# Performance work log

Hardware: AMD Instinct MI355X
Metric: run time of the kernel (lower is better)

The kernel has to match this reference:

```python
import jax, jax.numpy as jnp
import numpy as np

V, N, D, R, L, KS = 32000, 2048, 1024, 16, 4, 7
B, H = 2, 4 * 1024
GMIN, GMAX, ACAP = 0.85, 1.0, 1.0


def rmsnorm(x, w, eps=1e-6):
    return x * jax.lax.rsqrt(jnp.mean(x * x, axis=-1, keepdims=True) + eps) * w


def l2norm(x, eps=1e-8):
    return x / jnp.maximum(jnp.linalg.norm(x, axis=-1, keepdims=True), eps)


def mlp(x, w1, b1, w2, b2):
    return jax.nn.gelu(x @ w1 + b1) @ w2 + b2


def k1_block(h, nw, w1, b1, w2, b2):
    return h + mlp(rmsnorm(h, nw), w1, b1, w2, b2)


def causal_conv(h, kernel):
    # depthwise causal conv with shared 1D kernel; kernel[0] = current step
    n = h.shape[1]
    hp = jnp.pad(h, ((0, 0), (KS - 1, 0), (0, 0)))
    out = jnp.zeros_like(h)
    for k in range(KS):  # KS is small & static
        out = out + kernel[k] * hp[:, KS - 1 - k: KS - 1 - k + n, :]
    return out


def k2_layer(h, p):
    (u, v, dlog, alog, glog, kern, pw, pb, n1w, n2w, w1, b1, w2, b2) = p
    residual = h
    hn = rmsnorm(h, n1w)
    gate = jax.nn.sigmoid(glog)
    out = gate * causal_conv(hn, kern)
    # low-rank q/k
    q = l2norm(hn @ u)          # (B,N,R)
    k = l2norm(hn @ v)          # (B,N,R)
    gamma = GMIN + (GMAX - GMIN) * jax.nn.sigmoid(dlog)   # (R,)
    alpha = ACAP * jax.nn.sigmoid(alog)                   # (R,)
    qa = q * alpha
    pos = jnp.arange(h.shape[1])
    diff = jnp.maximum(pos[:, None] - pos[None, :], 0).astype(h.dtype)
    mask = (pos[:, None] >= pos[None, :]).astype(h.dtype)
    # per-rank causal decay matrix gamma_r^(i-j): (R,N,N)
    decay = jnp.exp(diff[None] * jnp.log(gamma)[:, None, None]) * mask[None]
    scores = jnp.einsum('bir,rij,bjr->bij', qa, decay, k)  # (B,N,N)
    out = out + jnp.einsum('bij,bjd->bid', scores, hn)
    out = out @ pw + pb
    h = residual + out
    h = h + mlp(rmsnorm(h, n2w), w1, b1, w2, b2)
    return h


def setup_inputs() -> dict:
    key = jax.random.key(0)
    ks = jax.random.split(key, 32)
    f32 = jnp.float32
    inp = {
        'tokens': jax.random.randint(ks[0], (B, N), 0, V),
        'emb_table': jax.random.normal(ks[1], (V, D), f32) * 0.02,
        'k1a_nw': jnp.ones((D,), f32),
        'k1a_w1': jax.random.normal(ks[2], (D, H), f32) * 0.02,
        'k1a_b1': jnp.zeros((H,), f32),
        'k1a_w2': jax.random.normal(ks[3], (H, D), f32) * 0.02,
        'k1a_b2': jnp.zeros((D,), f32),
        'k2_u': jax.random.normal(ks[4], (L, D, R), f32) * 0.05,
        'k2_v': jax.random.normal(ks[5], (L, D, R), f32) * 0.05,
        'k2_dlog': jax.random.normal(ks[6], (L, R), f32) * 0.5,
        'k2_alog': jnp.zeros((L, R), f32),
        'k2_glog': jnp.zeros((L,), f32),
        'k2_kern': jax.random.normal(ks[7], (L, KS), f32) * 0.1,
        'k2_pw': jax.random.normal(ks[8], (L, D, D), f32) * 0.02,
        'k2_pb': jnp.zeros((L, D), f32),
        'k2_n1w': jnp.ones((L, D), f32),
        'k2_n2w': jnp.ones((L, D), f32),
        'k2_w1': jax.random.normal(ks[9], (L, D, H), f32) * 0.02,
        'k2_b1': jnp.zeros((L, H), f32),
        'k2_w2': jax.random.normal(ks[10], (L, H, D), f32) * 0.02,
        'k2_b2': jnp.zeros((L, D), f32),
        'k1b_nw': jnp.ones((D,), f32),
        'k1b_w1': jax.random.normal(ks[11], (D, H), f32) * 0.02,
        'k1b_b1': jnp.zeros((H,), f32),
        'k1b_w2': jax.random.normal(ks[12], (H, D), f32) * 0.02,
        'k1b_b2': jnp.zeros((D,), f32),
        'k0_nw': jnp.ones((D,), f32),
        'head_w': jax.random.normal(ks[13], (D, V), f32) * 0.02,
        'head_b': jnp.zeros((V,), f32),
    }
    return inp


def reference(tokens, emb_table,
              k1a_nw, k1a_w1, k1a_b1, k1a_w2, k1a_b2,
              k2_u, k2_v, k2_dlog, k2_alog, k2_glog, k2_kern,
              k2_pw, k2_pb, k2_n1w, k2_n2w, k2_w1, k2_b1, k2_w2, k2_b2,
              k1b_nw, k1b_w1, k1b_b1, k1b_w2, k1b_b2,
              k0_nw, head_w, head_b):
    h = emb_table[tokens]                                  # (B,N,D)
    h = k1_block(h, k1a_nw, k1a_w1, k1a_b1, k1a_w2, k1a_b2)
    stacked = (k2_u, k2_v, k2_dlog, k2_alog, k2_glog, k2_kern,
               k2_pw, k2_pb, k2_n1w, k2_n2w, k2_w1, k2_b1, k2_w2, k2_b2)
    def step(c, p):
        return k2_layer(c, p), None
    h, _ = jax.lax.scan(step, h, stacked)
    h = k1_block(h, k1b_nw, k1b_w1, k1b_b1, k1b_w2, k1b_b2)
    h = rmsnorm(h, k0_nw)                                  # K0 final norm
    return h @ head_w + head_b                             # (B,N,V)
```

## Files before the change

### kernel.cpp

```cpp
#include <hip/hip_runtime.h>
#include <hip/hip_bf16.h>

#define SEQ 2048
#define DIM 1024
#define RNK 16
#define NL 4
#define KT 7
#define BATCH 2
#define HID 4096
#define VOC 32000
#define BNROWS (BATCH*SEQ)
#define CHK 128
#define NCH (SEQ/CHK)
#define PRMS 128
#define KAPP 160

typedef __hip_bfloat16 bf16;
typedef __attribute__((ext_vector_type(8))) short bh8;
typedef __attribute__((ext_vector_type(4))) float vf4;

__device__ __forceinline__ float bfu(unsigned int u) { u <<= 16; return __builtin_bit_cast(float, u); }
__device__ __forceinline__ unsigned short f2bu(float x) { bf16 t = __float2bfloat16(x); return __builtin_bit_cast(unsigned short, t); }
__device__ __forceinline__ float b2f(bf16 x) { return __bfloat162float(x); }
__device__ __forceinline__ float sigm(float x) { return 1.f / (1.f + expf(-x)); }
__device__ __forceinline__ float gelu_t(float x) {
    float u = 0.7978845608028654f * (x + 0.044715f * x * x * x);
    return 0.5f * x * (1.f + tanhf(u));
}

__device__ __forceinline__ void gld16(const bf16* g, bf16* l) {
    __builtin_amdgcn_global_load_lds(
        (const __attribute__((address_space(1))) void*)g,
        (__attribute__((address_space(3))) void*)l,
        16, 0, 0);
}

__global__ void embed_kernel(const int* __restrict__ tokens, const float* __restrict__ emb,
                             float* __restrict__ h) {
    int row = blockIdx.x;
    int tok = tokens[row];
    const float4* src = (const float4*)(emb + (size_t)tok * DIM);
    float4* dst = (float4*)(h + (size_t)row * DIM);
    dst[threadIdx.x] = src[threadIdx.x];
}

__global__ void rmsnorm_kernel(const float* __restrict__ in, const float* __restrict__ wt,
                               bf16* __restrict__ out) {
    int row = blockIdx.x;
    int tx = threadIdx.x;
    float4 v = ((const float4*)(in + (size_t)row * DIM))[tx];
    float ss = v.x * v.x + v.y * v.y + v.z * v.z + v.w * v.w;
#pragma unroll
    for (int off = 32; off > 0; off >>= 1) ss += __shfl_down(ss, off);
    __shared__ float red[4];
    int lane = tx & 63, wv = tx >> 6;
    if (lane == 0) red[wv] = ss;
    __syncthreads();
    float tot = red[0] + red[1] + red[2] + red[3];
    float scale = rsqrtf(tot * (1.f / DIM) + 1e-6f);
    float4 w4 = ((const float4*)wt)[tx];
    uint2 o;
    o.x = f2bu(v.x * scale * w4.x) | ((unsigned int)f2bu(v.y * scale * w4.y) << 16);
    o.y = f2bu(v.z * scale * w4.z) | ((unsigned int)f2bu(v.w * scale * w4.w) << 16);
    *(uint2*)(out + (size_t)row * DIM + tx * 4) = o;
}

__global__ void transpose_cast_kernel(const float* __restrict__ in, bf16* __restrict__ out,
                                      int K, int Nc) {
    __shared__ float tile[32][33];
    int n0 = blockIdx.x * 32, k0 = blockIdx.y * 32;
    int tx = threadIdx.x & 31, ty = threadIdx.x >> 5;
#pragma unroll
    for (int i = 0; i < 32; i += 8)
        tile[ty + i][tx] = in[(size_t)(k0 + ty + i) * Nc + n0 + tx];
    __syncthreads();
#pragma unroll
    for (int i = 0; i < 32; i += 8)
        out[(size_t)(n0 + ty + i) * K + k0 + tx] = __float2bfloat16(tile[tx][ty + i]);
}

__global__ void prep_kernel(const float* __restrict__ dlog, const float* __restrict__ alog,
                            const float* __restrict__ glog, const float* __restrict__ kern,
                            float* __restrict__ prm) {
    int l = blockIdx.x, t = threadIdx.x;
    float* p = prm + l * PRMS;
    if (t < RNK) {
        float g = 0.85f + 0.15f * sigm(dlog[l * RNK + t]);
        float lg = logf(g);
        p[t] = g;
        p[16 + t] = lg;
        p[32 + t] = expf(lg * (float)CHK);
        p[48 + t] = sigm(alog[l * RNK + t]);
    }
    if (t < KT) {
        float gate = sigm(glog[l]);
        p[64 + t] = gate * kern[l * KT + t];
    }
}

__global__ void prep_uv_kernel(const float* __restrict__ u, const float* __restrict__ v,
                               bf16* __restrict__ uvT) {
    int l = blockIdx.y;
    int k = blockIdx.x * 256 + threadIdx.x;
    const float* ul = u + (size_t)l * DIM * RNK;
    const float* vl = v + (size_t)l * DIM * RNK;
    bf16* o = uvT + (size_t)l * 32 * DIM;
#pragma unroll
    for (int r = 0; r < RNK; ++r) {
        o[(size_t)r * DIM + k] = __float2bfloat16(ul[(size_t)k * RNK + r]);
        o[(size_t)(RNK + r) * DIM + k] = __float2bfloat16(vl[(size_t)k * RNK + r]);
    }
}

__global__ void conv_kernel(const bf16* __restrict__ hn, const float* __restrict__ prm,
                            float* __restrict__ Z) {
    int t = blockIdx.x * 256 + threadIdx.x;
    int d4 = (t & 255) * 4;
    int row = t >> 8;
    int n = row & (SEQ - 1);
    float a0 = 0, a1 = 0, a2 = 0, a3 = 0;
#pragma unroll
    for (int kk = 0; kk < KT; ++kk) {
        if (n - kk < 0) break;
        float wv = prm[64 + kk];
        uint2 hv = *(const uint2*)(hn + (size_t)(row - kk) * DIM + d4);
        a0 += wv * bfu(hv.x & 0xffffu);
        a1 += wv * bfu(hv.x >> 16);
        a2 += wv * bfu(hv.y & 0xffffu);
        a3 += wv * bfu(hv.y >> 16);
    }
    float4 o = {a0, a1, a2, a3};
    *(float4*)(Z + (size_t)row * DIM + d4) = o;
}

__global__ __launch_bounds__(64)
void qk_mfma_kernel(const bf16* __restrict__ hn, const bf16* __restrict__ uvT,
                    const float* __restrict__ prm, float* __restrict__ qa,
                    float* __restrict__ kn) {
    int row0 = blockIdx.x * 32;
    int lane = threadIdx.x;
    int fr = lane & 15, kf = (lane >> 4) * 8;
    vf4 acc[2][2] = {};
#pragma unroll 4
    for (int kt = 0; kt < DIM / 32; ++kt) {
        int k0 = kt * 32;
        bh8 b0 = *(const bh8*)(uvT + (size_t)fr * DIM + k0 + kf);
        bh8 b1 = *(const bh8*)(uvT + (size_t)(16 + fr) * DIM + k0 + kf);
        bh8 a0 = *(const bh8*)(hn + (size_t)(row0 + fr) * DIM + k0 + kf);
        bh8 a1 = *(const bh8*)(hn + (size_t)(row0 + 16 + fr) * DIM + k0 + kf);
        acc[0][0] = __builtin_amdgcn_mfma_f32_16x16x32_bf16(a0, b0, acc[0][0], 0, 0, 0);
        acc[0][1] = __builtin_amdgcn_mfma_f32_16x16x32_bf16(a0, b1, acc[0][1], 0, 0, 0);
        acc[1][0] = __builtin_amdgcn_mfma_f32_16x16x32_bf16(a1, b0, acc[1][0], 0, 0, 0);
        acc[1][1] = __builtin_amdgcn_mfma_f32_16x16x32_bf16(a1, b1, acc[1][1], 0, 0, 0);
    }
    int fq = lane >> 4;
    float alpha = prm[48 + fr];
#pragma unroll
    for (int m = 0; m < 2; ++m) {
#pragma unroll
        for (int j = 0; j < 4; ++j) {
            float qv = acc[m][0][j], kv = acc[m][1][j];
            float sq = qv * qv, sk = kv * kv;
#pragma unroll
            for (int mask = 1; mask < 16; mask <<= 1) {
                sq += __shfl_xor(sq, mask);
                sk += __shfl_xor(sk, mask);
            }
            int row = row0 + m * 16 + fq * 4 + j;
            qa[(size_t)row * RNK + fr] = qv / fmaxf(sqrtf(sq), 1e-8f) * alpha;
            kn[(size_t)row * RNK + fr] = kv / fmaxf(sqrtf(sk), 1e-8f);
        }
    }
}

__global__ void trans_hn_kernel(const bf16* __restrict__ hn, bf16* __restrict__ HB) {
    __shared__ bf16 tile[32][40];
    int bc = blockIdx.x;
    int d0 = blockIdx.y * 32, j0 = blockIdx.z * 32;
    int tx = threadIdx.x & 31, ty = threadIdx.x >> 5;
    size_t rowb = (size_t)bc * CHK;
#pragma unroll
    for (int i = 0; i < 32; i += 8)
        tile[ty + i][tx] = hn[(rowb + j0 + ty + i) * DIM + d0 + tx];
    __syncthreads();
    bf16* Hp = HB + (size_t)bc * DIM * KAPP;
#pragma unroll
    for (int i = 0; i < 32; i += 8)
        Hp[(size_t)(d0 + ty + i) * KAPP + j0 + tx] = tile[tx][ty + i];
}

__global__ void scores_kernel(const float* __restrict__ qa, const float* __restrict__ kn,
                              const float* __restrict__ prm, bf16* __restrict__ SA,
                              bf16* __restrict__ kdtB) {
    int bc = blockIdx.x;
    __shared__ float ptab[CHK][16];
    for (int e = threadIdx.x; e < CHK * 16; e += 256) {
        int tt = e >> 4, r = e & 15;
        ptab[tt][r] = expf(prm[16 + r] * (float)tt);
    }
    __syncthreads();
    size_t rowb = (size_t)bc * CHK;
    bf16* SAp = SA + (size_t)bc * CHK * KAPP;
    for (int e = threadIdx.x; e < CHK * CHK; e += 256) {
        int i = e >> 7, j = e & (CHK - 1);
        float vsum = 0.f;
        if (i >= j) {
            const float* qp = qa + (rowb + i) * RNK;
            const float* kp = kn + (rowb + j) * RNK;
#pragma unroll
            for (int r = 0; r < 16; ++r) vsum += qp[r] * ptab[i - j][r] * kp[r];
        }
        SAp[(size_t)i * KAPP + j] = __float2bfloat16(vsum);
    }
    for (int e = threadIdx.x; e < CHK * 32; e += 256) {
        int i = e >> 5, rr = e & 31;
        float w = 0.f;
        if (rr < 16) w = qa[(rowb + i) * RNK + rr] * expf(prm[16 + rr] * (float)(i + 1));
        SAp[(size_t)i * KAPP + CHK + rr] = __float2bfloat16(w);
    }
    bf16* kp2 = kdtB + (size_t)bc * RNK * CHK;
    for (int e = threadIdx.x; e < RNK * CHK; e += 256) {
        int r = e >> 7, j = e & (CHK - 1);
        kp2[e] = __float2bfloat16(ptab[CHK - 1 - j][r] * kn[(rowb + j) * RNK + r]);
    }
}

__global__ __launch_bounds__(64)
void chunkU_kernel(const bf16* __restrict__ HB, const bf16* __restrict__ kdtB,
                   float* __restrict__ U) {
    int bc = blockIdx.x;
    int d0 = blockIdx.y * 64;
    int lane = threadIdx.x;
    int fr = lane & 15, kf = (lane >> 4) * 8;
    const bf16* Hp = HB + (size_t)bc * DIM * KAPP;
    const bf16* Kp = kdtB + (size_t)bc * RNK * CHK;
    vf4 acc[4] = {};
#pragma unroll
    for (int kt = 0; kt < 4; ++kt) {
        int k0 = kt * 32;
        bh8 bb = *(const bh8*)(Kp + (size_t)fr * CHK + k0 + kf);
#pragma unroll
        for (int m = 0; m < 4; ++m) {
            bh8 a = *(const bh8*)(Hp + (size_t)(d0 + m * 16 + fr) * KAPP + k0 + kf);
            acc[m] = __builtin_amdgcn_mfma_f32_16x16x32_bf16(a, bb, acc[m], 0, 0, 0);
        }
    }
    int fq = lane >> 4;
    float* Up = U + (size_t)bc * DIM * RNK;
#pragma unroll
    for (int m = 0; m < 4; ++m)
#pragma unroll
        for (int j = 0; j < 4; ++j)
            Up[(size_t)(d0 + m * 16 + fq * 4 + j) * RNK + fr] = acc[m][j];
}

__global__ void scanP_kernel(const float* __restrict__ U, const float* __restrict__ prm,
                             bf16* __restrict__ HB) {
    int g = blockIdx.x * 256 + threadIdx.x;
    int d = g & (DIM - 1);
    int b = g >> 10;
    float gC[16], p[16];
#pragma unroll
    for (int r = 0; r < 16; ++r) { gC[r] = prm[32 + r]; p[r] = 0.f; }
    for (int c = 0; c < NCH; ++c) {
        int bc = b * NCH + c;
        unsigned int pk[8];
#pragma unroll
        for (int q = 0; q < 8; ++q)
            pk[q] = (unsigned int)f2bu(p[2 * q]) | ((unsigned int)f2bu(p[2 * q + 1]) << 16);
        uint4* dst = (uint4*)(HB + (size_t)bc * DIM * KAPP + (size_t)d * KAPP + CHK);
        dst[0] = make_uint4(pk[0], pk[1], pk[2], pk[3]);
        dst[1] = make_uint4(pk[4], pk[5], pk[6], pk[7]);
        const float4* up = (const float4*)(U + ((size_t)bc * DIM + d) * RNK);
#pragma unroll
        for (int q = 0; q < 4; ++q) {
            float4 u4 = up[q];
            p[4 * q + 0] = gC[4 * q + 0] * p[4 * q + 0] + u4.x;
            p[4 * q + 1] = gC[4 * q + 1] * p[4 * q + 1] + u4.y;
            p[4 * q + 2] = gC[4 * q + 2] * p[4 * q + 2] + u4.z;
            p[4 * q + 3] = gC[4 * q + 3] * p[4 * q + 3] + u4.w;
        }
    }
}

__global__ __launch_bounds__(256)
void apply_gemm_kernel(const bf16* __restrict__ SA, const bf16* __restrict__ HB,
                       const float* __restrict__ Z, bf16* __restrict__ Zb) {
    __shared__ alignas(16) bf16 As[128][40];
    __shared__ alignas(16) bf16 Bs[128][40];
    int bc = blockIdx.y;
    int colB0 = blockIdx.x * 128;
    int t = threadIdx.x;
    int lane = t & 63, wid = t >> 6;
    int wr = wid >> 1, wc = wid & 1;
    vf4 acc[4][4] = {};
    const bf16* A = SA + (size_t)bc * CHK * KAPP;
    const bf16* BT = HB + (size_t)bc * DIM * KAPP;
    int r1 = t >> 2, ko1 = (t & 3) * 8;
    int fr = lane & 15, kf = (lane >> 4) * 8;
#pragma unroll
    for (int kt = 0; kt < 5; ++kt) {
        int k0 = kt * 32;
        int4 va1 = *(const int4*)(A + (size_t)r1 * KAPP + k0 + ko1);
        int4 va2 = *(const int4*)(A + (size_t)(r1 + 64) * KAPP + k0 + ko1);
        int4 vb1 = *(const int4*)(BT + (size_t)(colB0 + r1) * KAPP + k0 + ko1);
        int4 vb2 = *(const int4*)(BT + (size_t)(colB0 + r1 + 64) * KAPP + k0 + ko1);
        __syncthreads();
        *(int4*)&As[r1][ko1] = va1;
        *(int4*)&As[r1 + 64][ko1] = va2;
        *(int4*)&Bs[r1][ko1] = vb1;
        *(int4*)&Bs[r1 + 64][ko1] = vb2;
        __syncthreads();
        bh8 a[4], bb[4];
#pragma unroll
        for (int m = 0; m < 4; ++m) a[m] = *(const bh8*)&As[wr * 64 + m * 16 + fr][kf];
#pragma unroll
        for (int n = 0; n < 4; ++n) bb[n] = *(const bh8*)&Bs[wc * 64 + n * 16 + fr][kf];
#pragma unroll
        for (int m = 0; m < 4; ++m)
#pragma unroll
            for (int n = 0; n < 4; ++n)
                acc[m][n] = __builtin_amdgcn_mfma_f32_16x16x32_bf16(a[m], bb[n], acc[m][n], 0, 0, 0);
    }
    int fq = lane >> 4;
    size_t rowb = (size_t)bc * CHK;
#pragma unroll
    for (int m = 0; m < 4; ++m) {
#pragma unroll
        for (int n = 0; n < 4; ++n) {
            int col = colB0 + wc * 64 + n * 16 + fr;
#pragma unroll
            for (int j = 0; j < 4; ++j) {
                size_t row = rowb + wr * 64 + m * 16 + fq * 4 + j;
                size_t idx = row * DIM + col;
                Zb[idx] = __float2bfloat16(Z[idx] + acc[m][n][j]);
            }
        }
    }
}

template <int EPI>
__global__ __launch_bounds__(256)
void gemm_kernel(const bf16* __restrict__ A, const bf16* __restrict__ BT,
                 const float* __restrict__ bias, const float* __restrict__ res,
                 float* __restrict__ outF, bf16* __restrict__ outB,
                 int M, int Nc, int K, int lda) {
    __shared__ alignas(16) bf16 As[128][32];
    __shared__ alignas(16) bf16 Bs[128][32];
    int gx = gridDim.x;
    int orig = blockIdx.y * gx + blockIdx.x;
    int qch = (gx * gridDim.y) >> 3;
    int wg = (orig & 7) * qch + (orig >> 3);
    int bn = wg % gx, bm = wg / gx;
    int t = threadIdx.x;
    int lane = t & 63, wid = t >> 6;
    int wr = wid >> 1, wc = wid & 1;
    vf4 acc[4][4] = {};
    const int rowA0 = bm * 128, colB0 = bn * 128;
    int fr = lane & 15, kf = (lane >> 4) * 8;
    int c0 = wid * 2;
    int lrow = lane >> 2;
    int lcol = (lane & 3) * 8;
    const bf16* Ag0 = A + (size_t)(rowA0 + c0 * 16 + lrow) * lda + lcol;
    const bf16* Ag1 = A + (size_t)(rowA0 + c0 * 16 + 16 + lrow) * lda + lcol;
    const bf16* Bg0 = BT + (size_t)(colB0 + c0 * 16 + lrow) * lda + lcol;
    const bf16* Bg1 = BT + (size_t)(colB0 + c0 * 16 + 16 + lrow) * lda + lcol;
    bf16* Al0 = &As[0][0] + c0 * 512;
    bf16* Al1 = Al0 + 512;
    bf16* Bl0 = &Bs[0][0] + c0 * 512;
    bf16* Bl1 = Bl0 + 512;
    int nk = K >> 5;
    for (int kt = 0; kt < nk; ++kt) {
        int k0 = kt * 32;
        __syncthreads();
        gld16(Ag0 + k0, Al0);
        gld16(Ag1 + k0, Al1);
        gld16(Bg0 + k0, Bl0);
        gld16(Bg1 + k0, Bl1);
        asm volatile("s_waitcnt vmcnt(0)" ::: "memory");
        __syncthreads();
        bh8 a[4], bb[4];
#pragma unroll
        for (int m = 0; m < 4; ++m) a[m] = *(const bh8*)&As[wr * 64 + m * 16 + fr][kf];
#pragma unroll
        for (int n = 0; n < 4; ++n) bb[n] = *(const bh8*)&Bs[wc * 64 + n * 16 + fr][kf];
#pragma unroll
        for (int m = 0; m < 4; ++m)
#pragma unroll
            for (int n = 0; n < 4; ++n)
                acc[m][n] = __builtin_amdgcn_mfma_f32_16x16x32_bf16(a[m], bb[n], acc[m][n], 0, 0, 0);
    }
    int fq = lane >> 4;
#pragma unroll
    for (int m = 0; m < 4; ++m) {
#pragma unroll
        for (int n = 0; n < 4; ++n) {
            int col = colB0 + wc * 64 + n * 16 + fr;
            float bv = bias[col];
#pragma unroll
            for (int j = 0; j < 4; ++j) {
                int row = rowA0 + wr * 64 + m * 16 + fq * 4 + j;
                size_t idx = (size_t)row * Nc + col;
                float v2 = acc[m][n][j] + bv;
                if (EPI == 1) v2 += res[idx];
                outF[idx] = v2;
            }
        }
    }
}

#define SB __builtin_amdgcn_sched_barrier(0)
template <int EPI>
__global__ __launch_bounds__(512, 2)
void gemm256_kernel(const bf16* __restrict__ A, const bf16* __restrict__ BT,
                    const float* __restrict__ bias,
                    float* __restrict__ outF, bf16* __restrict__ outB,
                    int M, int Nc, int K, int lda) {
    extern __shared__ char smem[];
    bf16* Alds = (bf16*)smem;
    bf16* Blds = (bf16*)(smem + 65536);
    if (EPI == 3) {
        size_t zo = (size_t)blockIdx.z * K;
        A += zo; BT += zo;
        outF += (size_t)blockIdx.z * ((size_t)M * Nc);
    }
    int gx = gridDim.x, gy = gridDim.y;
    int orig = blockIdx.y * gx + blockIdx.x;
    int qch = (gx * gy) >> 3;
    int wg = (orig & 7) * qch + (orig >> 3);
    int bm = wg % gy, bn = wg / gy;
    int rowA0 = bm * 256, colB0 = bn * 256;
    int tid = threadIdx.x;
    int lane = tid & 63, wid = tid >> 6;
    int wm = wid >> 2, wn = wid & 3;
    int fr = lane & 15;
    int kf8 = ((((lane >> 4) & 3) ^ ((fr >> 1) & 3)) * 8);
    int srow = wid * 16 + (lane >> 2);
    int scol = (((lane & 3) ^ ((lane >> 3) & 3)) * 8);
    const bf16* Ags = A + (size_t)(rowA0 + srow) * lda + scol;
    const bf16* Bgs = BT + (size_t)(colB0 + srow) * lda + scol;
    int sbase = wid * 512;
    auto stA = [&](int d, int kh, int k0) {
        bf16* dst = Alds + (d * 2 + kh) * 8192 + sbase;
        const bf16* src = Ags + k0 + kh * 32;
        gld16(src, dst);
        gld16(src + (size_t)128 * lda, dst + 4096);
    };
    auto stB = [&](int d, int kh, int k0) {
        bf16* dst = Blds + (d * 2 + kh) * 8192 + sbase;
        const bf16* src = Bgs + k0 + kh * 32;
        gld16(src, dst);
        gld16(src + (size_t)128 * lda, dst + 4096);
    };
    const bf16* Ard = Alds + (size_t)(wm * 128 + fr) * 32 + kf8;
    const bf16* Brd = Blds + (size_t)(wn * 64 + fr) * 32 + kf8;
    vf4 acc[8][4] = {};
    int nt = K >> 6;
    stA(0, 0, 0); stB(0, 0, 0); stA(0, 1, 0); stB(0, 1, 0);
    for (int t = 0; t < nt; ++t) {
        int d = t & 1, nd = d ^ 1;
        int k1 = (t + 1) << 6;
        bool pf = (t + 1 < nt);
        int dof = d * 16384;
        bh8 bF[4];
        if (pf) { stA(nd, 0, k1); asm volatile("s_waitcnt vmcnt(6)" ::: "memory"); }
        else    {                 asm volatile("s_waitcnt vmcnt(4)" ::: "memory"); }
        SB; __builtin_amdgcn_s_barrier(); SB;
        {
            bh8 a0 = *(const bh8*)(Ard + dof + 0 * 512);
            bh8 a1 = *(const bh8*)(Ard + dof + 1 * 512);
            bh8 a2 = *(const bh8*)(Ard + dof + 2 * 512);
            bh8 a3 = *(const bh8*)(Ard + dof + 3 * 512);
#pragma unroll
            for (int n = 0; n < 4; ++n) bF[n] = *(const bh8*)(Brd + dof + n * 512);
            __builtin_amdgcn_s_setprio(1);
#pragma unroll
            for (int n = 0; n < 4; ++n) {
                acc[0][n] = __builtin_amdgcn_mfma_f32_16x16x32_bf16(a0, bF[n], acc[0][n], 0, 0, 0);
                acc[1][n] = __builtin_amdgcn_mfma_f32_16x16x32_bf16(a1, bF[n], acc[1][n], 0, 0, 0);
                acc[2][n] = __builtin_amdgcn_mfma_f32_16x16x32_bf16(a2, bF[n], acc[2][n], 0, 0, 0);
                acc[3][n] = __builtin_amdgcn_mfma_f32_16x16x32_bf16(a3, bF[n], acc[3][n], 0, 0, 0);
            }
            __builtin_amdgcn_s_setprio(0);
        }
        SB;
        if (pf) stB(nd, 0, k1);
        SB; __builtin_amdgcn_s_barrier(); SB;
        {
            bh8 a0 = *(const bh8*)(Ard + dof + 4 * 512);
            bh8 a1 = *(const bh8*)(Ard + dof + 5 * 512);
            bh8 a2 = *(const bh8*)(Ard + dof + 6 * 512);
            bh8 a3 = *(const bh8*)(Ard + dof + 7 * 512);
            __builtin_amdgcn_s_setprio(1);
#pragma unroll
            for (int n = 0; n < 4; ++n) {
                acc[4][n] = __builtin_amdgcn_mfma_f32_16x16x32_bf16(a0, bF[n], acc[4][n], 0, 0, 0);
                acc[5][n] = __builtin_amdgcn_mfma_f32_16x16x32_bf16(a1, bF[n], acc[5][n], 0, 0, 0);
                acc[6][n] = __builtin_amdgcn_mfma_f32_16x16x32_bf16(a2, bF[n], acc[6][n], 0, 0, 0);
                acc[7][n] = __builtin_amdgcn_mfma_f32_16x16x32_bf16(a3, bF[n], acc[7][n], 0, 0, 0);
            }
            __builtin_amdgcn_s_setprio(0);
        }
        SB;
        int dof1 = dof + 8192;
        if (pf) { stA(nd, 1, k1); asm volatile("s_waitcnt vmcnt(6)" ::: "memory"); }
        else    {                 asm volatile("s_waitcnt vmcnt(0)" ::: "memory"); }
        SB; __builtin_amdgcn_s_barrier(); SB;
        {
            bh8 a0 = *(const bh8*)(Ard + dof1 + 0 * 512);
            bh8 a1 = *(const bh8*)(Ard + dof1 + 1 * 512);
            bh8 a2 = *(const bh8*)(Ard + dof1 + 2 * 512);
            bh8 a3 = *(const bh8*)(Ard + dof1 + 3 * 512);
#pragma unroll
            for (int n = 0; n < 4; ++n) bF[n] = *(const bh8*)(Brd + dof1 + n * 512);
            __builtin_amdgcn_s_setprio(1);
#pragma unroll
            for (int n = 0; n < 4; ++n) {
                acc[0][n] = __builtin_amdgcn_mfma_f32_16x16x32_bf16(a0, bF[n], acc[0][n], 0, 0, 0);
                acc[1][n] = __builtin_amdgcn_mfma_f32_16x16x32_bf16(a1, bF[n], acc[1][n], 0, 0, 0);
                acc[2][n] = __builtin_amdgcn_mfma_f32_16x16x32_bf16(a2, bF[n], acc[2][n], 0, 0, 0);
                acc[3][n] = __builtin_amdgcn_mfma_f32_16x16x32_bf16(a3, bF[n], acc[3][n], 0, 0, 0);
            }
            __builtin_amdgcn_s_setprio(0);
        }
        SB;
        if (pf) stB(nd, 1, k1);
        SB; __builtin_amdgcn_s_barrier(); SB;
        {
            bh8 a0 = *(const bh8*)(Ard + dof1 + 4 * 512);
            bh8 a1 = *(const bh8*)(Ard + dof1 + 5 * 512);
            bh8 a2 = *(const bh8*)(Ard + dof1 + 6 * 512);
            bh8 a3 = *(const bh8*)(Ard + dof1 + 7 * 512);
            __builtin_amdgcn_s_setprio(1);
#pragma unroll
            for (int n = 0; n < 4; ++n) {
                acc[4][n] = __builtin_amdgcn_mfma_f32_16x16x32_bf16(a0, bF[n], acc[4][n], 0, 0, 0);
                acc[5][n] = __builtin_amdgcn_mfma_f32_16x16x32_bf16(a1, bF[n], acc[5][n], 0, 0, 0);
                acc[6][n] = __builtin_amdgcn_mfma_f32_16x16x32_bf16(a2, bF[n], acc[6][n], 0, 0, 0);
                acc[7][n] = __builtin_amdgcn_mfma_f32_16x16x32_bf16(a3, bF[n], acc[7][n], 0, 0, 0);
            }
            __builtin_amdgcn_s_setprio(0);
        }
        SB;
    }
    int fq = lane >> 4;
#pragma unroll
    for (int mi = 0; mi < 8; ++mi) {
#pragma unroll
        for (int ni = 0; ni < 4; ++ni) {
            int col = colB0 + wn * 64 + ni * 16 + fr;
            float bv = (EPI == 3) ? 0.f : bias[col];
#pragma unroll
            for (int j = 0; j < 4; ++j) {
                int row = rowA0 + wm * 128 + mi * 16 + fq * 4 + j;
                size_t idx = (size_t)row * Nc + col;
                float v2 = acc[mi][ni][j] + bv;
                if (EPI == 2) outB[idx] = __float2bfloat16(gelu_t(v2));
                else outF[idx] = v2;
            }
        }
    }
}

__global__ void combine4_norm_kernel(const float* __restrict__ P, const float* __restrict__ bias,
                                     const float* __restrict__ nw, float* __restrict__ h,
                                     bf16* __restrict__ hnb) {
    int row = blockIdx.x;
    int tx = threadIdx.x;
    int t = row * 256 + tx;
    const size_t S = (size_t)BNROWS * DIM;
    float4 p0 = ((const float4*)P)[t];
    float4 p1 = ((const float4*)(P + S))[t];
    float4 p2 = ((const float4*)(P + 2 * S))[t];
    float4 p3 = ((const float4*)(P + 3 * S))[t];
    float4 bv = ((const float4*)bias)[tx];
    float4 hv = ((float4*)h)[t];
    hv.x += (p0.x + p1.x) + (p2.x + p3.x) + bv.x;
    hv.y += (p0.y + p1.y) + (p2.y + p3.y) + bv.y;
    hv.z += (p0.z + p1.z) + (p2.z + p3.z) + bv.z;
    hv.w += (p0.w + p1.w) + (p2.w + p3.w) + bv.w;
    ((float4*)h)[t] = hv;
    float ss = hv.x * hv.x + hv.y * hv.y + hv.z * hv.z + hv.w * hv.w;
#pragma unroll
    for (int off = 32; off > 0; off >>= 1) ss += __shfl_down(ss, off);
    __shared__ float red[4];
    int lane = tx & 63, wv = tx >> 6;
    if (lane == 0) red[wv] = ss;
    __syncthreads();
    float tot = red[0] + red[1] + red[2] + red[3];
    float scale = rsqrtf(tot * (1.f / DIM) + 1e-6f);
    float4 w4 = ((const float4*)nw)[tx];
    uint2 o;
    o.x = f2bu(hv.x * scale * w4.x) | ((unsigned int)f2bu(hv.y * scale * w4.y) << 16);
    o.y = f2bu(hv.z * scale * w4.z) | ((unsigned int)f2bu(hv.w * scale * w4.w) << 16);
    *(uint2*)(hnb + (size_t)row * DIM + tx * 4) = o;
}

extern "C" void kernel_launch(void* const* d_in, const int* in_sizes, int n_in,
                              void* d_out, int out_size, void* d_ws, size_t ws_size,
                              hipStream_t stream) {
    (void)in_sizes; (void)n_in; (void)out_size; (void)ws_size;
    const int* tokens = (const int*)d_in[0];
    const float* emb = (const float*)d_in[1];
    const float* k1a_nw = (const float*)d_in[2];
    const float* k1a_w1 = (const float*)d_in[3];
    const float* k1a_b1 = (const float*)d_in[4];
    const float* k1a_w2 = (const float*)d_in[5];
    const float* k1a_b2 = (const float*)d_in[6];
    const float* k2_u = (const float*)d_in[7];
    const float* k2_v = (const float*)d_in[8];
    const float* k2_dlog = (const float*)d_in[9];
    const float* k2_alog = (const float*)d_in[10];
    const float* k2_glog = (const float*)d_in[11];
    const float* k2_kern = (const float*)d_in[12];
    const float* k2_pw = (const float*)d_in[13];
    const float* k2_pb = (const float*)d_in[14];
    const float* k2_n1w = (const float*)d_in[15];
    const float* k2_n2w = (const float*)d_in[16];
    const float* k2_w1 = (const float*)d_in[17];
    const float* k2_b1 = (const float*)d_in[18];
    const float* k2_w2 = (const float*)d_in[19];
    const float* k2_b2 = (const float*)d_in[20];
    const float* k1b_nw = (const float*)d_in[21];
    const float* k1b_w1 = (const float*)d_in[22];
    const float* k1b_b1 = (const float*)d_in[23];
    const float* k1b_w2 = (const float*)d_in[24];
    const float* k1b_b2 = (const float*)d_in[25];
    const float* k0_nw = (const float*)d_in[26];
    const float* head_w = (const float*)d_in[27];
    const float* head_b = (const float*)d_in[28];
    float* out = (float*)d_out;

    (void)hipFuncSetAttribute((const void*)gemm256_kernel<0>,
                              hipFuncAttributeMaxDynamicSharedMemorySize, 131072);
    (void)hipFuncSetAttribute((const void*)gemm256_kernel<2>,
                              hipFuncAttributeMaxDynamicSharedMemorySize, 131072);
    (void)hipFuncSetAttribute((const void*)gemm256_kernel<3>,
                              hipFuncAttributeMaxDynamicSharedMemorySize, 131072);

    char* wsp = (char*)d_ws;
    auto alloc = [&](size_t bytes) -> char* {
        char* p = wsp;
        wsp += (bytes + 255) & ~(size_t)255;
        return p;
    };
    float* h   = (float*)alloc((size_t)BNROWS * DIM * 4);
    float* Z   = (float*)alloc((size_t)BNROWS * DIM * 4);
    bf16* hnb  = (bf16*)alloc((size_t)BNROWS * DIM * 2);
    bf16* Zb   = (bf16*)alloc((size_t)BNROWS * DIM * 2);
    bf16* t1b  = (bf16*)alloc((size_t)BNROWS * HID * 2);
    float* qaB = (float*)alloc((size_t)BNROWS * RNK * 4);
    float* knB = (float*)alloc((size_t)BNROWS * RNK * 4);
    float* U   = (float*)alloc((size_t)BATCH * NCH * DIM * RNK * 4);
    bf16* HB   = (bf16*)alloc((size_t)BATCH * NCH * DIM * KAPP * 2);
    bf16* SA   = (bf16*)alloc((size_t)BATCH * NCH * CHK * KAPP * 2);
    bf16* kdtB = (bf16*)alloc((size_t)BATCH * NCH * RNK * CHK * 2);
    float* prm = (float*)alloc((size_t)NL * PRMS * 4);
    bf16* uvT  = (bf16*)alloc((size_t)NL * 32 * DIM * 2);
    bf16* w1aT = (bf16*)alloc((size_t)HID * DIM * 2);
    bf16* w2aT = (bf16*)alloc((size_t)DIM * HID * 2);
    bf16* w1bT = (bf16*)alloc((size_t)HID * DIM * 2);
    bf16* w2bT = (bf16*)alloc((size_t)DIM * HID * 2);
    bf16* pwT  = (bf16*)alloc((size_t)NL * DIM * DIM * 2);
    bf16* w1T  = (bf16*)alloc((size_t)NL * DIM * HID * 2);
    bf16* w2T  = (bf16*)alloc((size_t)NL * HID * DIM * 2);
    bf16* headT = (bf16*)alloc((size_t)VOC * DIM * 2);
    float* Pk  = (float*)alloc((size_t)4 * BNROWS * DIM * 4);

    hipMemsetAsync(HB, 0, (size_t)BATCH * NCH * DIM * KAPP * 2, stream);

    auto T = [&](const float* in, bf16* o, int K, int Nc) {
        transpose_cast_kernel<<<dim3(Nc / 32, K / 32), 256, 0, stream>>>(in, o, K, Nc);
    };
    T(k1a_w1, w1aT, DIM, HID);
    T(k1a_w2, w2aT, HID, DIM);
    T(k1b_w1, w1bT, DIM, HID);
    T(k1b_w2, w2bT, HID, DIM);
    for (int l = 0; l < NL; ++l) {
        T(k2_pw + (size_t)l * DIM * DIM, pwT + (size_t)l * DIM * DIM, DIM, DIM);
        T(k2_w1 + (size_t)l * DIM * HID, w1T + (size_t)l * DIM * HID, DIM, HID);
        T(k2_w2 + (size_t)l * HID * DIM, w2T + (size_t)l * HID * DIM, HID, DIM);
    }
    T(head_w, headT, DIM, VOC);
    prep_kernel<<<NL, 32, 0, stream>>>(k2_dlog, k2_alog, k2_glog, k2_kern, prm);
    prep_uv_kernel<<<dim3(DIM / 256, NL), 256, 0, stream>>>(k2_u, k2_v, uvT);

    auto mlp_core = [&](const bf16* W1, const float* B1, const bf16* W2, const float* B2,
                        const float* nw_next) {
        gemm256_kernel<2><<<dim3(HID / 256, BNROWS / 256), 512, 131072, stream>>>(
            hnb, W1, B1, nullptr, t1b, BNROWS, HID, DIM, DIM);
        gemm256_kernel<3><<<dim3(DIM / 256, BNROWS / 256, 4), 512, 131072, stream>>>(
            t1b, W2, nullptr, Pk, nullptr, BNROWS, DIM, HID / 4, HID);
        combine4_norm_kernel<<<BNROWS, 256, 0, stream>>>(Pk, B2, nw_next, h, hnb);
    };

    embed_kernel<<<BNROWS, 256, 0, stream>>>(tokens, emb, h);
    rmsnorm_kernel<<<BNROWS, 256, 0, stream>>>(h, k1a_nw, hnb);
    mlp_core(w1aT, k1a_b1, w2aT, k1a_b2, k2_n1w);

    for (int l = 0; l < NL; ++l) {
        const float* prm_l = prm + l * PRMS;
        conv_kernel<<<BNROWS, 256, 0, stream>>>(hnb, prm_l, Z);
        qk_mfma_kernel<<<BNROWS / 32, 64, 0, stream>>>(hnb, uvT + (size_t)l * 32 * DIM,
                                                       prm_l, qaB, knB);
        trans_hn_kernel<<<dim3(BATCH * NCH, DIM / 32, CHK / 32), 256, 0, stream>>>(hnb, HB);
        scores_kernel<<<BATCH * NCH, 256, 0, stream>>>(qaB, knB, prm_l, SA, kdtB);
        chunkU_kernel<<<dim3(BATCH * NCH, DIM / 64), 64, 0, stream>>>(HB, kdtB, U);
        scanP_kernel<<<BATCH * DIM / 256, 256, 0, stream>>>(U, prm_l, HB);
        apply_gemm_kernel<<<dim3(DIM / 128, BATCH * NCH), 256, 0, stream>>>(SA, HB, Z, Zb);
        gemm_kernel<1><<<dim3(DIM / 128, BNROWS / 128), 256, 0, stream>>>(
            Zb, pwT + (size_t)l * DIM * DIM, k2_pb + (size_t)l * DIM, h, h, nullptr,
            BNROWS, DIM, DIM, DIM);
        rmsnorm_kernel<<<BNROWS, 256, 0, stream>>>(h, k2_n2w + (size_t)l * DIM, hnb);
        const float* nw_next = (l < NL - 1) ? (k2_n1w + (size_t)(l + 1) * DIM) : k1b_nw;
        mlp_core(w1T + (size_t)l * DIM * HID, k2_b1 + (size_t)l * HID,
                 w2T + (size_t)l * HID * DIM, k2_b2 + (size_t)l * DIM, nw_next);
    }

    mlp_core(w1bT, k1b_b1, w2bT, k1b_b2, k0_nw);

    gemm256_kernel<0><<<dim3(VOC / 256, BNROWS / 256), 512, 131072, stream>>>(
        hnb, headT, head_b, out, nullptr, BNROWS, VOC, DIM, DIM);
}
```

Measured before the change: 1.711 ms.

## Store split-K partials in bf16 and widen grids of small scan/score kernels

Split-K partial sums of the second MLP GEMM are now written as bf16 instead of fp32, and the combine kernel reads them that way, halving partial-buffer traffic at some cost in accuracy. The qk, scores and scanP kernels are also split across more blocks or threads (16-row qk tiles, 8 row-slices per chunk for scores, 4 rank-groups per d in scanP) to raise parallelism on these previously under-occupied launches. This adds redundant ptab setup per scores block and lowers per-wave work and reuse in qk.

```diff
diff --git a/kernel.cpp b/kernel.cpp
--- a/kernel.cpp
+++ b/kernel.cpp
@@ -137,39 +137,33 @@
 void qk_mfma_kernel(const bf16* __restrict__ hn, const bf16* __restrict__ uvT,
                     const float* __restrict__ prm, float* __restrict__ qa,
                     float* __restrict__ kn) {
-    int row0 = blockIdx.x * 32;
+    int row0 = blockIdx.x * 16;
     int lane = threadIdx.x;
     int fr = lane & 15, kf = (lane >> 4) * 8;
-    vf4 acc[2][2] = {};
+    vf4 accq = {}, acck = {};
 #pragma unroll 4
     for (int kt = 0; kt < DIM / 32; ++kt) {
         int k0 = kt * 32;
         bh8 b0 = *(const bh8*)(uvT + (size_t)fr * DIM + k0 + kf);
         bh8 b1 = *(const bh8*)(uvT + (size_t)(16 + fr) * DIM + k0 + kf);
         bh8 a0 = *(const bh8*)(hn + (size_t)(row0 + fr) * DIM + k0 + kf);
-        bh8 a1 = *(const bh8*)(hn + (size_t)(row0 + 16 + fr) * DIM + k0 + kf);
-        acc[0][0] = __builtin_amdgcn_mfma_f32_16x16x32_bf16(a0, b0, acc[0][0], 0, 0, 0);
-        acc[0][1] = __builtin_amdgcn_mfma_f32_16x16x32_bf16(a0, b1, acc[0][1], 0, 0, 0);
-        acc[1][0] = __builtin_amdgcn_mfma_f32_16x16x32_bf16(a1, b0, acc[1][0], 0, 0, 0);
-        acc[1][1] = __builtin_amdgcn_mfma_f32_16x16x32_bf16(a1, b1, acc[1][1], 0, 0, 0);
+        accq = __builtin_amdgcn_mfma_f32_16x16x32_bf16(a0, b0, accq, 0, 0, 0);
+        acck = __builtin_amdgcn_mfma_f32_16x16x32_bf16(a0, b1, acck, 0, 0, 0);
     }
     int fq = lane >> 4;
     float alpha = prm[48 + fr];
 #pragma unroll
-    for (int m = 0; m < 2; ++m) {
-#pragma unroll
-        for (int j = 0; j < 4; ++j) {
-            float qv = acc[m][0][j], kv = acc[m][1][j];
-            float sq = qv * qv, sk = kv * kv;
-#pragma unroll
-            for (int mask = 1; mask < 16; mask <<= 1) {
-                sq += __shfl_xor(sq, mask);
-                sk += __shfl_xor(sk, mask);
-            }
-            int row = row0 + m * 16 + fq * 4 + j;
-            qa[(size_t)row * RNK + fr] = qv / fmaxf(sqrtf(sq), 1e-8f) * alpha;
-            kn[(size_t)row * RNK + fr] = kv / fmaxf(sqrtf(sk), 1e-8f);
-        }
+    for (int j = 0; j < 4; ++j) {
+        float qv = accq[j], kv = acck[j];
+        float sq = qv * qv, sk = kv * kv;
+#pragma unroll
+        for (int mask = 1; mask < 16; mask <<= 1) {
+            sq += __shfl_xor(sq, mask);
+            sk += __shfl_xor(sk, mask);
+        }
+        int row = row0 + fq * 4 + j;
+        qa[(size_t)row * RNK + fr] = qv / fmaxf(sqrtf(sq), 1e-8f) * alpha;
+        kn[(size_t)row * RNK + fr] = kv / fmaxf(sqrtf(sk), 1e-8f);
     }
 }
 
@@ -193,6 +187,7 @@
                               const float* __restrict__ prm, bf16* __restrict__ SA,
                               bf16* __restrict__ kdtB) {
     int bc = blockIdx.x;
+    int yt = blockIdx.y;
     __shared__ float ptab[CHK][16];
     for (int e = threadIdx.x; e < CHK * 16; e += 256) {
         int tt = e >> 4, r = e & 15;
@@ -201,8 +196,8 @@
     __syncthreads();
     size_t rowb = (size_t)bc * CHK;
     bf16* SAp = SA + (size_t)bc * CHK * KAPP;
-    for (int e = threadIdx.x; e < CHK * CHK; e += 256) {
-        int i = e >> 7, j = e & (CHK - 1);
+    for (int e = threadIdx.x; e < 16 * CHK; e += 256) {
+        int i = yt * 16 + (e >> 7), j = e & (CHK - 1);
         float vsum = 0.f;
         if (i >= j) {
             const float* qp = qa + (rowb + i) * RNK;
@@ -212,16 +207,17 @@
         }
         SAp[(size_t)i * KAPP + j] = __float2bfloat16(vsum);
     }
-    for (int e = threadIdx.x; e < CHK * 32; e += 256) {
-        int i = e >> 5, rr = e & 31;
+    for (int e = threadIdx.x; e < 16 * 32; e += 256) {
+        int i = yt * 16 + (e >> 5), rr = e & 31;
         float w = 0.f;
         if (rr < 16) w = qa[(rowb + i) * RNK + rr] * expf(prm[16 + rr] * (float)(i + 1));
         SAp[(size_t)i * KAPP + CHK + rr] = __float2bfloat16(w);
     }
     bf16* kp2 = kdtB + (size_t)bc * RNK * CHK;
-    for (int e = threadIdx.x; e < RNK * CHK; e += 256) {
-        int r = e >> 7, j = e & (CHK - 1);
-        kp2[e] = __float2bfloat16(ptab[CHK - 1 - j][r] * kn[(rowb + j) * RNK + r]);
+    for (int e = threadIdx.x; e < 2 * CHK; e += 256) {
+        int r = 2 * yt + (e >> 7), j = e & (CHK - 1);
+        kp2[(size_t)r * CHK + j] =
+            __float2bfloat16(ptab[CHK - 1 - j][r] * kn[(rowb + j) * RNK + r]);
     }
 }
 
@@ -257,29 +253,23 @@
 __global__ void scanP_kernel(const float* __restrict__ U, const float* __restrict__ prm,
                              bf16* __restrict__ HB) {
     int g = blockIdx.x * 256 + threadIdx.x;
-    int d = g & (DIM - 1);
-    int b = g >> 10;
-    float gC[16], p[16];
-#pragma unroll
-    for (int r = 0; r < 16; ++r) { gC[r] = prm[32 + r]; p[r] = 0.f; }
+    int rq = g & 3;
+    int d = (g >> 2) & (DIM - 1);
+    int b = g >> 12;
+    float gC[4], p[4];
+#pragma unroll
+    for (int q = 0; q < 4; ++q) { gC[q] = prm[32 + rq * 4 + q]; p[q] = 0.f; }
     for (int c = 0; c < NCH; ++c) {
         int bc = b * NCH + c;
-        unsigned int pk[8];
-#pragma unroll
-        for (int q = 0; q < 8; ++q)
-            pk[q] = (unsigned int)f2bu(p[2 * q]) | ((unsigned int)f2bu(p[2 * q + 1]) << 16);
-        uint4* dst = (uint4*)(HB + (size_t)bc * DIM * KAPP + (size_t)d * KAPP + CHK);
-        dst[0] = make_uint4(pk[0], pk[1], pk[2], pk[3]);
-        dst[1] = make_uint4(pk[4], pk[5], pk[6], pk[7]);
-        const float4* up = (const float4*)(U + ((size_t)bc * DIM + d) * RNK);
-#pragma unroll
-        for (int q = 0; q < 4; ++q) {
-            float4 u4 = up[q];
-            p[4 * q + 0] = gC[4 * q + 0] * p[4 * q + 0] + u4.x;
-            p[4 * q + 1] = gC[4 * q + 1] * p[4 * q + 1] + u4.y;
-            p[4 * q + 2] = gC[4 * q + 2] * p[4 * q + 2] + u4.z;
-            p[4 * q + 3] = gC[4 * q + 3] * p[4 * q + 3] + u4.w;
-        }
+        uint2 pk;
+        pk.x = (unsigned int)f2bu(p[0]) | ((unsigned int)f2bu(p[1]) << 16);
+        pk.y = (unsigned int)f2bu(p[2]) | ((unsigned int)f2bu(p[3]) << 16);
+        *(uint2*)(HB + (size_t)bc * DIM * KAPP + (size_t)d * KAPP + CHK + rq * 4) = pk;
+        float4 u4 = *(const float4*)(U + ((size_t)bc * DIM + d) * RNK + rq * 4);
+        p[0] = gC[0] * p[0] + u4.x;
+        p[1] = gC[1] * p[1] + u4.y;
+        p[2] = gC[2] * p[2] + u4.z;
+        p[3] = gC[3] * p[3] + u4.w;
     }
 }
 
@@ -419,10 +409,10 @@
     extern __shared__ char smem[];
     bf16* Alds = (bf16*)smem;
     bf16* Blds = (bf16*)(smem + 65536);
-    if (EPI == 3) {
+    if (EPI == 4) {
         size_t zo = (size_t)blockIdx.z * K;
         A += zo; BT += zo;
-        outF += (size_t)blockIdx.z * ((size_t)M * Nc);
+        outB += (size_t)blockIdx.z * ((size_t)M * Nc);
     }
     int gx = gridDim.x, gy = gridDim.y;
     int orig = blockIdx.y * gx + blockIdx.x;
@@ -549,37 +539,40 @@
 #pragma unroll
         for (int ni = 0; ni < 4; ++ni) {
             int col = colB0 + wn * 64 + ni * 16 + fr;
-            float bv = (EPI == 3) ? 0.f : bias[col];
+            float bv = (EPI == 4) ? 0.f : bias[col];
 #pragma unroll
             for (int j = 0; j < 4; ++j) {
                 int row = rowA0 + wm * 128 + mi * 16 + fq * 4 + j;
                 size_t idx = (size_t)row * Nc + col;
                 float v2 = acc[mi][ni][j] + bv;
                 if (EPI == 2) outB[idx] = __float2bfloat16(gelu_t(v2));
+                else if (EPI == 4) outB[idx] = __float2bfloat16(v2);
                 else outF[idx] = v2;
             }
         }
     }
 }
 
-__global__ void combine4_norm_kernel(const float* __restrict__ P, const float* __restrict__ bias,
+__global__ void combine4_norm_kernel(const bf16* __restrict__ P, const float* __restrict__ bias,
                                      const float* __restrict__ nw, float* __restrict__ h,
                                      bf16* __restrict__ hnb) {
     int row = blockIdx.x;
     int tx = threadIdx.x;
-    int t = row * 256 + tx;
     const size_t S = (size_t)BNROWS * DIM;
-    float4 p0 = ((const float4*)P)[t];
-    float4 p1 = ((const float4*)(P + S))[t];
-    float4 p2 = ((const float4*)(P + 2 * S))[t];
-    float4 p3 = ((const float4*)(P + 3 * S))[t];
+    size_t base = (size_t)row * DIM + tx * 4;
+    float4 hv = *(float4*)(h + base);
     float4 bv = ((const float4*)bias)[tx];
-    float4 hv = ((float4*)h)[t];
-    hv.x += (p0.x + p1.x) + (p2.x + p3.x) + bv.x;
-    hv.y += (p0.y + p1.y) + (p2.y + p3.y) + bv.y;
-    hv.z += (p0.z + p1.z) + (p2.z + p3.z) + bv.z;
-    hv.w += (p0.w + p1.w) + (p2.w + p3.w) + bv.w;
-    ((float4*)h)[t] = hv;
+    float s0 = bv.x, s1 = bv.y, s2 = bv.z, s3 = bv.w;
+#pragma unroll
+    for (int q = 0; q < 4; ++q) {
+        uint2 pk = *(const uint2*)(P + q * S + base);
+        s0 += bfu(pk.x & 0xffffu);
+        s1 += bfu(pk.x >> 16);
+        s2 += bfu(pk.y & 0xffffu);
+        s3 += bfu(pk.y >> 16);
+    }
+    hv.x += s0; hv.y += s1; hv.z += s2; hv.w += s3;
+    *(float4*)(h + base) = hv;
     float ss = hv.x * hv.x + hv.y * hv.y + hv.z * hv.z + hv.w * hv.w;
 #pragma unroll
     for (int off = 32; off > 0; off >>= 1) ss += __shfl_down(ss, off);
@@ -635,7 +628,7 @@
                               hipFuncAttributeMaxDynamicSharedMemorySize, 131072);
     (void)hipFuncSetAttribute((const void*)gemm256_kernel<2>,
                               hipFuncAttributeMaxDynamicSharedMemorySize, 131072);
-    (void)hipFuncSetAttribute((const void*)gemm256_kernel<3>,
+    (void)hipFuncSetAttribute((const void*)gemm256_kernel<4>,
                               hipFuncAttributeMaxDynamicSharedMemorySize, 131072);
 
     char* wsp = (char*)d_ws;
@@ -665,7 +658,7 @@
     bf16* w1T  = (bf16*)alloc((size_t)NL * DIM * HID * 2);
     bf16* w2T  = (bf16*)alloc((size_t)NL * HID * DIM * 2);
     bf16* headT = (bf16*)alloc((size_t)VOC * DIM * 2);
-    float* Pk  = (float*)alloc((size_t)4 * BNROWS * DIM * 4);
+    bf16* Pk  = (bf16*)alloc((size_t)4 * BNROWS * DIM * 2);
 
     hipMemsetAsync(HB, 0, (size_t)BATCH * NCH * DIM * KAPP * 2, stream);
 
@@ -689,8 +682,8 @@
                         const float* nw_next) {
         gemm256_kernel<2><<<dim3(HID / 256, BNROWS / 256), 512, 131072, stream>>>(
             hnb, W1, B1, nullptr, t1b, BNROWS, HID, DIM, DIM);
-        gemm256_kernel<3><<<dim3(DIM / 256, BNROWS / 256, 4), 512, 131072, stream>>>(
-            t1b, W2, nullptr, Pk, nullptr, BNROWS, DIM, HID / 4, HID);
+        gemm256_kernel<4><<<dim3(DIM / 256, BNROWS / 256, 4), 512, 131072, stream>>>(
+            t1b, W2, nullptr, nullptr, Pk, BNROWS, DIM, HID / 4, HID);
         combine4_norm_kernel<<<BNROWS, 256, 0, stream>>>(Pk, B2, nw_next, h, hnb);
     };
 
@@ -701,12 +694,12 @@
     for (int l = 0; l < NL; ++l) {
         const float* prm_l = prm + l * PRMS;
         conv_kernel<<<BNROWS, 256, 0, stream>>>(hnb, prm_l, Z);
-        qk_mfma_kernel<<<BNROWS / 32, 64, 0, stream>>>(hnb, uvT + (size_t)l * 32 * DIM,
+        qk_mfma_kernel<<<BNROWS / 16, 64, 0, stream>>>(hnb, uvT + (size_t)l * 32 * DIM,
                                                        prm_l, qaB, knB);
         trans_hn_kernel<<<dim3(BATCH * NCH, DIM / 32, CHK / 32), 256, 0, stream>>>(hnb, HB);
-        scores_kernel<<<BATCH * NCH, 256, 0, stream>>>(qaB, knB, prm_l, SA, kdtB);
+        scores_kernel<<<dim3(BATCH * NCH, 8), 256, 0, stream>>>(qaB, knB, prm_l, SA, kdtB);
         chunkU_kernel<<<dim3(BATCH * NCH, DIM / 64), 64, 0, stream>>>(HB, kdtB, U);
-        scanP_kernel<<<BATCH * DIM / 256, 256, 0, stream>>>(U, prm_l, HB);
+        scanP_kernel<<<BATCH * DIM * 4 / 256, 256, 0, stream>>>(U, prm_l, HB);
         apply_gemm_kernel<<<dim3(DIM / 128, BATCH * NCH), 256, 0, stream>>>(SA, HB, Z, Zb);
         gemm_kernel<1><<<dim3(DIM / 128, BNROWS / 128), 256, 0, stream>>>(
             Zb, pwT + (size_t)l * DIM * DIM, k2_pb + (size_t)l * DIM, h, h, nullptr,
```

After: 1.546 ms. 1.11x faster.
